# Optimization experiments

Hardware: AMD Instinct MI355X
Metric: run time of the kernel (lower is better)

The kernel has to match this reference:

```python
import jax, jax.numpy as jnp
import numpy as np

MARGIN = 0.1
SQUARED = False
EPS = 1e-16


def pairwise_distance(emb, squared=False):
    # emb: [N, D]
    dot = emb @ emb.T                      # [N, N]
    sq = jnp.diagonal(dot)                 # [N]
    d = sq[:, None] - 2.0 * dot + sq[None, :]
    d = jnp.maximum(d, 0.0)
    if not squared:
        zero = (d == 0.0).astype(d.dtype)
        d = jnp.sqrt(d + zero * EPS)       # eps keeps grad finite at 0
        d = d * (1.0 - zero)
    return d


def get_triplet_mask(labels):
    n = labels.shape[0]
    neq = ~jnp.eye(n, dtype=bool)
    distinct = neq[:, :, None] & neq[:, None, :] & neq[None, :, :]
    lbl_eq = labels[:, None] == labels[None, :]
    valid = lbl_eq[:, :, None] & (~lbl_eq)[:, None, :]
    return distinct & valid


def setup_inputs() -> dict:
    key = jax.random.key(0)
    k1, k2 = jax.random.split(key)
    embeddings = jax.random.normal(k1, (512, 256), dtype=jnp.float32)
    labels = jax.random.randint(k2, (512,), 0, 32, dtype=jnp.int64 if jax.config.jax_enable_x64 else jnp.int32)
    return {"embeddings": embeddings, "labels": labels}


def reference(embeddings, labels):
    pd = pairwise_distance(embeddings, squared=SQUARED)        # [N, N]
    # anchor-positive dist [N,N,1] minus anchor-negative dist [N,1,N]
    triplet_loss = pd[:, :, None] - pd[:, None, :] + MARGIN     # [N, N, N]
    mask = get_triplet_mask(labels).astype(triplet_loss.dtype)
    triplet_loss = jax.nn.relu(triplet_loss * mask)
    num_hard = jnp.sum((triplet_loss > EPS).astype(triplet_loss.dtype))
    loss = jnp.sum(triplet_loss) / (num_hard + EPS)
    return loss, num_hard
```

## Files before the change

kernel.cpp:

```cpp
#include <hip/hip_runtime.h>
#include <hip/hip_bf16.h>

#define N 512
#define D 256
#define MARGIN 0.1f
#define EPSF 1e-16f

#define PAD 4
__global__ __launch_bounds__(256) void pd_kernel(const float* __restrict__ E,
                                                 float* __restrict__ pd) {
    __shared__ float As[32][D + PAD];
    __shared__ float Bs[32][D + PAD];
    __shared__ float norms[64];
    int bi = blockIdx.y, bj = blockIdx.x;
    int t = threadIdx.x;

    const float4* E4 = (const float4*)E;
    #pragma unroll
    for (int it = 0; it < 8; ++it) {
        int idx = it * 256 + t;
        int r = idx >> 6;
        int c = idx & 63;
        float4 va = E4[(bi * 32 + r) * 64 + c];
        *(float4*)&As[r][c * 4] = va;
        float4 vb = E4[(bj * 32 + r) * 64 + c];
        *(float4*)&Bs[r][c * 4] = vb;
    }
    __syncthreads();

    {
        int r  = t >> 2;
        int ch = t & 3;
        const float* src = (r < 32) ? &As[r][0] : &Bs[r - 32][0];
        float np = 0.0f;
        #pragma unroll
        for (int d = 0; d < 64; d += 4) {
            float4 x = *(const float4*)&src[ch * 64 + d];
            np += x.x * x.x + x.y * x.y + x.z * x.z + x.w * x.w;
        }
        np += __shfl_xor(np, 1);
        np += __shfl_xor(np, 2);
        if (ch == 0) norms[r] = np;
    }
    __syncthreads();

    int ri = t >> 4;
    int cj = t & 15;
    float a00 = 0.f, a01 = 0.f, a10 = 0.f, a11 = 0.f;
    for (int d = 0; d < D; d += 4) {
        float4 x0 = *(const float4*)&As[ri][d];
        float4 x1 = *(const float4*)&As[ri + 16][d];
        float4 y0 = *(const float4*)&Bs[cj][d];
        float4 y1 = *(const float4*)&Bs[cj + 16][d];
        a00 += x0.x * y0.x + x0.y * y0.y + x0.z * y0.z + x0.w * y0.w;
        a01 += x0.x * y1.x + x0.y * y1.y + x0.z * y1.z + x0.w * y1.w;
        a10 += x1.x * y0.x + x1.y * y0.y + x1.z * y0.z + x1.w * y0.w;
        a11 += x1.x * y1.x + x1.y * y1.y + x1.z * y1.z + x1.w * y1.w;
    }

    int gi0 = bi * 32 + ri, gi1 = gi0 + 16;
    int gj0 = bj * 32 + cj, gj1 = gj0 + 16;
    float si0 = norms[ri],      si1 = norms[ri + 16];
    float sj0 = norms[32 + cj], sj1 = norms[32 + cj + 16];

    {
        float dd = si0 - 2.0f * a00 + sj0;
        dd = fmaxf(dd, 0.0f);
        pd[gi0 * N + gj0] = (dd > 0.0f) ? sqrtf(dd) : 0.0f;
    }
    {
        float dd = si0 - 2.0f * a01 + sj1;
        dd = fmaxf(dd, 0.0f);
        pd[gi0 * N + gj1] = (dd > 0.0f) ? sqrtf(dd) : 0.0f;
    }
    {
        float dd = si1 - 2.0f * a10 + sj0;
        dd = fmaxf(dd, 0.0f);
        pd[gi1 * N + gj0] = (dd > 0.0f) ? sqrtf(dd) : 0.0f;
    }
    {
        float dd = si1 - 2.0f * a11 + sj1;
        dd = fmaxf(dd, 0.0f);
        pd[gi1 * N + gj1] = (dd > 0.0f) ? sqrtf(dd) : 0.0f;
    }
}

__global__ __launch_bounds__(256) void triplet_kernel(const float* __restrict__ pd,
                                                      const int* __restrict__ labels,
                                                      float* __restrict__ bsum,
                                                      float* __restrict__ bcnt) {
    __shared__ float row[N];
    __shared__ int   lab[N];
    __shared__ unsigned long long masks[8];
    __shared__ short plist[N];
    __shared__ float ssum[256];
    __shared__ int   scnt[256];

    int i = blockIdx.x;
    int t = threadIdx.x;
    int wave = t >> 6;
    int lane = t & 63;

    row[t]       = pd[i * N + t];
    row[t + 256] = pd[i * N + t + 256];
    lab[t]       = labels[t];
    lab[t + 256] = labels[t + 256];
    __syncthreads();

    int li = lab[i];
    int j1 = t, j2 = t + 256;
    bool p1 = (lab[j1] == li) && (j1 != i);
    bool p2 = (lab[j2] == li) && (j2 != i);
    unsigned long long m1 = __ballot(p1);
    unsigned long long m2 = __ballot(p2);
    if (lane == 0) { masks[wave] = m1; masks[wave + 4] = m2; }
    __syncthreads();

    int base1 = 0, base2 = 0, npos = 0;
    #pragma unroll
    for (int c = 0; c < 8; ++c) {
        int pc = __popcll(masks[c]);
        if (c < wave)     base1 += pc;
        if (c < wave + 4) base2 += pc;
        npos += pc;
    }
    unsigned long long lower = (1ULL << lane) - 1ULL;
    if (p1) plist[base1 + __popcll(m1 & lower)] = (short)j1;
    if (p2) plist[base2 + __popcll(m2 & lower)] = (short)j2;
    __syncthreads();

    bool  n1  = (lab[j1] != li);
    bool  n2  = (lab[j2] != li);
    float dn1 = row[j1];
    float dn2 = row[j2];

    float sum = 0.0f;
    int cnt = 0;
    for (int p = 0; p < npos; ++p) {
        float dap = row[plist[p]];
        float v1 = dap - dn1 + MARGIN;
        float v2 = dap - dn2 + MARGIN;
        if (n1 && v1 > 0.0f) { sum += v1; cnt += (v1 > EPSF); }
        if (n2 && v2 > 0.0f) { sum += v2; cnt += (v2 > EPSF); }
    }

    ssum[t] = sum;
    scnt[t] = cnt;
    __syncthreads();
    #pragma unroll
    for (int s = 128; s > 0; s >>= 1) {
        if (t < s) {
            ssum[t] += ssum[t + s];
            scnt[t] += scnt[t + s];
        }
        __syncthreads();
    }
    if (t == 0) {
        bsum[i] = ssum[0];
        bcnt[i] = (float)scnt[0];
    }
}

__global__ __launch_bounds__(256) void final_kernel(const float* __restrict__ bsum,
                                                    const float* __restrict__ bcnt,
                                                    float* __restrict__ out) {
    __shared__ double s[256];
    __shared__ double c[256];
    int t = threadIdx.x;
    s[t] = (double)bsum[t] + (double)bsum[t + 256];
    c[t] = (double)bcnt[t] + (double)bcnt[t + 256];
    __syncthreads();
    #pragma unroll
    for (int st = 128; st > 0; st >>= 1) {
        if (t < st) {
            s[t] += s[t + st];
            c[t] += c[t + st];
        }
        __syncthreads();
    }
    if (t == 0) {
        double cnt = c[0];
        out[0] = (float)(s[0] / (cnt + 1e-16));
        out[1] = (float)cnt;
    }
}

extern "C" void kernel_launch(void* const* d_in, const int* in_sizes, int n_in,
                              void* d_out, int out_size, void* d_ws, size_t ws_size,
                              hipStream_t stream) {
    const float* E      = (const float*)d_in[0];
    const int*   labels = (const int*)d_in[1];
    float* out = (float*)d_out;

    float* pd   = (float*)d_ws;
    float* bsum = pd + N * N;
    float* bcnt = bsum + 512;

    pd_kernel<<<dim3(16, 16), 256, 0, stream>>>(E, pd);
    triplet_kernel<<<N, 256, 0, stream>>>(pd, labels, bsum, bcnt);
    final_kernel<<<1, 256, 0, stream>>>(bsum, bcnt, out);
}
```

Before: 18.07 us.

## Fuse pairwise distance computation into triplet kernel, two anchor rows per block

Drops the separate pairwise-distance kernel and the N×N distance matrix in global memory. Each of 256 blocks now handles two anchor rows, computing their distance rows directly from the embeddings (dot products plus recomputed squared norms) in shared memory before running the triplet reduction. This removes one launch and the distance-matrix round trip. In exchange every block reads the full 512×256 embedding matrix from global/L2, so the GEMM work is redone with low reuse, and only 256 blocks run.

```diff
diff --git a/kernel.cpp b/kernel.cpp
--- a/kernel.cpp
+++ b/kernel.cpp
@@ -6,158 +6,134 @@
 #define MARGIN 0.1f
 #define EPSF 1e-16f
 
-#define PAD 4
-__global__ __launch_bounds__(256) void pd_kernel(const float* __restrict__ E,
-                                                 float* __restrict__ pd) {
-    __shared__ float As[32][D + PAD];
-    __shared__ float Bs[32][D + PAD];
-    __shared__ float norms[64];
-    int bi = blockIdx.y, bj = blockIdx.x;
-    int t = threadIdx.x;
-
-    const float4* E4 = (const float4*)E;
-    #pragma unroll
-    for (int it = 0; it < 8; ++it) {
-        int idx = it * 256 + t;
-        int r = idx >> 6;
-        int c = idx & 63;
-        float4 va = E4[(bi * 32 + r) * 64 + c];
-        *(float4*)&As[r][c * 4] = va;
-        float4 vb = E4[(bj * 32 + r) * 64 + c];
-        *(float4*)&Bs[r][c * 4] = vb;
-    }
-    __syncthreads();
-
-    {
-        int r  = t >> 2;
-        int ch = t & 3;
-        const float* src = (r < 32) ? &As[r][0] : &Bs[r - 32][0];
-        float np = 0.0f;
-        #pragma unroll
-        for (int d = 0; d < 64; d += 4) {
-            float4 x = *(const float4*)&src[ch * 64 + d];
-            np += x.x * x.x + x.y * x.y + x.z * x.z + x.w * x.w;
-        }
-        np += __shfl_xor(np, 1);
-        np += __shfl_xor(np, 2);
-        if (ch == 0) norms[r] = np;
-    }
-    __syncthreads();
-
-    int ri = t >> 4;
-    int cj = t & 15;
-    float a00 = 0.f, a01 = 0.f, a10 = 0.f, a11 = 0.f;
-    for (int d = 0; d < D; d += 4) {
-        float4 x0 = *(const float4*)&As[ri][d];
-        float4 x1 = *(const float4*)&As[ri + 16][d];
-        float4 y0 = *(const float4*)&Bs[cj][d];
-        float4 y1 = *(const float4*)&Bs[cj + 16][d];
-        a00 += x0.x * y0.x + x0.y * y0.y + x0.z * y0.z + x0.w * y0.w;
-        a01 += x0.x * y1.x + x0.y * y1.y + x0.z * y1.z + x0.w * y1.w;
-        a10 += x1.x * y0.x + x1.y * y0.y + x1.z * y0.z + x1.w * y0.w;
-        a11 += x1.x * y1.x + x1.y * y1.y + x1.z * y1.z + x1.w * y1.w;
-    }
-
-    int gi0 = bi * 32 + ri, gi1 = gi0 + 16;
-    int gj0 = bj * 32 + cj, gj1 = gj0 + 16;
-    float si0 = norms[ri],      si1 = norms[ri + 16];
-    float sj0 = norms[32 + cj], sj1 = norms[32 + cj + 16];
-
-    {
-        float dd = si0 - 2.0f * a00 + sj0;
-        dd = fmaxf(dd, 0.0f);
-        pd[gi0 * N + gj0] = (dd > 0.0f) ? sqrtf(dd) : 0.0f;
-    }
-    {
-        float dd = si0 - 2.0f * a01 + sj1;
-        dd = fmaxf(dd, 0.0f);
-        pd[gi0 * N + gj1] = (dd > 0.0f) ? sqrtf(dd) : 0.0f;
-    }
-    {
-        float dd = si1 - 2.0f * a10 + sj0;
-        dd = fmaxf(dd, 0.0f);
-        pd[gi1 * N + gj0] = (dd > 0.0f) ? sqrtf(dd) : 0.0f;
-    }
-    {
-        float dd = si1 - 2.0f * a11 + sj1;
-        dd = fmaxf(dd, 0.0f);
-        pd[gi1 * N + gj1] = (dd > 0.0f) ? sqrtf(dd) : 0.0f;
-    }
-}
-
-__global__ __launch_bounds__(256) void triplet_kernel(const float* __restrict__ pd,
-                                                      const int* __restrict__ labels,
-                                                      float* __restrict__ bsum,
-                                                      float* __restrict__ bcnt) {
-    __shared__ float row[N];
+__global__ __launch_bounds__(256) void row_triplet_kernel(const float* __restrict__ E,
+                                                          const int* __restrict__ labels,
+                                                          float* __restrict__ bsum,
+                                                          float* __restrict__ bcnt) {
+    __shared__ float rowA[D];
+    __shared__ float rowB[D];
+    __shared__ float sqv[N];
+    __shared__ float dr[2][N];
     __shared__ int   lab[N];
     __shared__ unsigned long long masks[8];
     __shared__ short plist[N];
     __shared__ float ssum[256];
     __shared__ int   scnt[256];
 
-    int i = blockIdx.x;
-    int t = threadIdx.x;
-    int wave = t >> 6;
-    int lane = t & 63;
+    int t   = threadIdx.x;
+    int blk = blockIdx.x;
+    int i0 = blk, i1 = blk + 256;
 
-    row[t]       = pd[i * N + t];
-    row[t + 256] = pd[i * N + t + 256];
+    const float4* E4 = (const float4*)E;
+
+    if (t < 64) {
+        *(float4*)&rowA[t * 4] = E4[i0 * 64 + t];
+    } else if (t < 128) {
+        int c = t - 64;
+        *(float4*)&rowB[c * 4] = E4[i1 * 64 + c];
+    }
     lab[t]       = labels[t];
     lab[t + 256] = labels[t + 256];
     __syncthreads();
 
-    int li = lab[i];
-    int j1 = t, j2 = t + 256;
-    bool p1 = (lab[j1] == li) && (j1 != i);
-    bool p2 = (lab[j2] == li) && (j2 != i);
-    unsigned long long m1 = __ballot(p1);
-    unsigned long long m2 = __ballot(p2);
-    if (lane == 0) { masks[wave] = m1; masks[wave + 4] = m2; }
+    int rl = t >> 2;
+    int ch = t & 3;
+    for (int p = 0; p < 8; ++p) {
+        int j = p * 64 + rl;
+        float dot0 = 0.f, dot1 = 0.f, sq = 0.f;
+        #pragma unroll
+        for (int k = 0; k < 16; ++k) {
+            int c = ch + 4 * k;
+            float4 x  = E4[j * 64 + c];
+            float4 va = *(const float4*)&rowA[c * 4];
+            float4 vb = *(const float4*)&rowB[c * 4];
+            dot0 += x.x * va.x + x.y * va.y + x.z * va.z + x.w * va.w;
+            dot1 += x.x * vb.x + x.y * vb.y + x.z * vb.z + x.w * vb.w;
+            sq   += x.x * x.x + x.y * x.y + x.z * x.z + x.w * x.w;
+        }
+        dot0 += __shfl_xor(dot0, 1);  dot0 += __shfl_xor(dot0, 2);
+        dot1 += __shfl_xor(dot1, 1);  dot1 += __shfl_xor(dot1, 2);
+        sq   += __shfl_xor(sq, 1);    sq   += __shfl_xor(sq, 2);
+        if (ch == 0) {
+            sqv[j]   = sq;
+            dr[0][j] = dot0;
+            dr[1][j] = dot1;
+        }
+    }
     __syncthreads();
 
-    int base1 = 0, base2 = 0, npos = 0;
+    float si0 = sqv[i0], si1 = sqv[i1];
     #pragma unroll
-    for (int c = 0; c < 8; ++c) {
-        int pc = __popcll(masks[c]);
-        if (c < wave)     base1 += pc;
-        if (c < wave + 4) base2 += pc;
-        npos += pc;
+    for (int a = 0; a < 2; ++a) {
+        int j = t + a * 256;
+        float sj  = sqv[j];
+        float dd0 = fmaxf(si0 - 2.0f * dr[0][j] + sj, 0.0f);
+        float dd1 = fmaxf(si1 - 2.0f * dr[1][j] + sj, 0.0f);
+        dr[0][j] = (dd0 > 0.0f) ? sqrtf(dd0) : 0.0f;
+        dr[1][j] = (dd1 > 0.0f) ? sqrtf(dd1) : 0.0f;
     }
-    unsigned long long lower = (1ULL << lane) - 1ULL;
-    if (p1) plist[base1 + __popcll(m1 & lower)] = (short)j1;
-    if (p2) plist[base2 + __popcll(m2 & lower)] = (short)j2;
     __syncthreads();
 
-    bool  n1  = (lab[j1] != li);
-    bool  n2  = (lab[j2] != li);
-    float dn1 = row[j1];
-    float dn2 = row[j2];
+    int wave = t >> 6;
+    int lane = t & 63;
+    unsigned long long lower = (1ULL << lane) - 1ULL;
 
-    float sum = 0.0f;
-    int cnt = 0;
-    for (int p = 0; p < npos; ++p) {
-        float dap = row[plist[p]];
-        float v1 = dap - dn1 + MARGIN;
-        float v2 = dap - dn2 + MARGIN;
-        if (n1 && v1 > 0.0f) { sum += v1; cnt += (v1 > EPSF); }
-        if (n2 && v2 > 0.0f) { sum += v2; cnt += (v2 > EPSF); }
-    }
+    for (int a = 0; a < 2; ++a) {
+        int i = (a == 0) ? i0 : i1;
+        const float* row = dr[a];
 
-    ssum[t] = sum;
-    scnt[t] = cnt;
-    __syncthreads();
-    #pragma unroll
-    for (int s = 128; s > 0; s >>= 1) {
-        if (t < s) {
-            ssum[t] += ssum[t + s];
-            scnt[t] += scnt[t + s];
+        int li = lab[i];
+        int j1 = t, j2 = t + 256;
+        bool p1 = (lab[j1] == li) && (j1 != i);
+        bool p2 = (lab[j2] == li) && (j2 != i);
+        unsigned long long m1 = __ballot(p1);
+        unsigned long long m2 = __ballot(p2);
+        if (lane == 0) { masks[wave] = m1; masks[wave + 4] = m2; }
+        __syncthreads();
+
+        int base1 = 0, base2 = 0, npos = 0;
+        #pragma unroll
+        for (int c = 0; c < 8; ++c) {
+            int pc = __popcll(masks[c]);
+            if (c < wave)     base1 += pc;
+            if (c < wave + 4) base2 += pc;
+            npos += pc;
+        }
+        if (p1) plist[base1 + __popcll(m1 & lower)] = (short)j1;
+        if (p2) plist[base2 + __popcll(m2 & lower)] = (short)j2;
+        __syncthreads();
+
+        bool  n1  = (lab[j1] != li);
+        bool  n2  = (lab[j2] != li);
+        float dn1 = row[j1];
+        float dn2 = row[j2];
+
+        float sum = 0.0f;
+        int cnt = 0;
+        for (int p = 0; p < npos; ++p) {
+            float dap = row[plist[p]];
+            float v1 = dap - dn1 + MARGIN;
+            float v2 = dap - dn2 + MARGIN;
+            if (n1 && v1 > 0.0f) { sum += v1; cnt += (v1 > EPSF); }
+            if (n2 && v2 > 0.0f) { sum += v2; cnt += (v2 > EPSF); }
+        }
+
+        ssum[t] = sum;
+        scnt[t] = cnt;
+        __syncthreads();
+        #pragma unroll
+        for (int s = 128; s > 0; s >>= 1) {
+            if (t < s) {
+                ssum[t] += ssum[t + s];
+                scnt[t] += scnt[t + s];
+            }
+            __syncthreads();
+        }
+        if (t == 0) {
+            bsum[i] = ssum[0];
+            bcnt[i] = (float)scnt[0];
         }
         __syncthreads();
-    }
-    if (t == 0) {
-        bsum[i] = ssum[0];
-        bcnt[i] = (float)scnt[0];
     }
 }
 
@@ -190,13 +166,11 @@
                               hipStream_t stream) {
     const float* E      = (const float*)d_in[0];
     const int*   labels = (const int*)d_in[1];
-    float* out = (float*)d_out;
+    float*       out    = (float*)d_out;
 
-    float* pd   = (float*)d_ws;
-    float* bsum = pd + N * N;
+    float* bsum = (float*)d_ws;
     float* bcnt = bsum + 512;
 
-    pd_kernel<<<dim3(16, 16), 256, 0, stream>>>(E, pd);
-    triplet_kernel<<<N, 256, 0, stream>>>(pd, labels, bsum, bcnt);
+    row_triplet_kernel<<<256, 256, 0, stream>>>(E, labels, bsum, bcnt);
     final_kernel<<<1, 256, 0, stream>>>(bsum, bcnt, out);
 }
```

New measurement: 29.43 us. 62.9% more time.
